# Performance work log

Hardware: AMD Instinct MI355X
Metric: run time of the kernel (lower is better)

Reference implementation:

```python
import jax, jax.numpy as jnp
import numpy as np
from jax import lax

L, H, D, HID, FF, S, B, IN = 2, 8, 64, 512, 2048, 256, 8, 512


def _self_ref(x, Wy, Wq, Wk, wb):
    # x: (B,H,S,D) already softmaxed; Wy/Wq/Wk: (B,H,D,D); wb: (B,H,D,4)
    # Self-referential weight matrix update (SRWM, self_ref_v0):
    #   y = Wy x; q = softmax(Wq x); k = softmax(Wk x); beta = sigmoid(wb^T x)
    #   W <- W + beta_W * (W q - W k) outer k   (one beta per sub-matrix)
    def step(carry, x_t):
        Wy, Wq, Wk, wb = carry
        y = jnp.einsum('bhij,bhj->bhi', Wy, x_t)
        q = jax.nn.softmax(jnp.einsum('bhij,bhj->bhi', Wq, x_t), axis=-1)
        k = jax.nn.softmax(jnp.einsum('bhij,bhj->bhi', Wk, x_t), axis=-1)
        beta = jax.nn.sigmoid(jnp.einsum('bhjc,bhj->bhc', wb, x_t))  # (B,H,4)
        d = q - k                                                    # W q - W k = W (q-k)
        dy = jnp.einsum('bhij,bhj->bhi', Wy, d)
        dq = jnp.einsum('bhij,bhj->bhi', Wq, d)
        dk = jnp.einsum('bhij,bhj->bhi', Wk, d)
        db = jnp.einsum('bhjc,bhj->bhc', wb, d)                      # (B,H,4)
        Wy = Wy + beta[..., 0, None, None] * dy[..., :, None] * k[..., None, :]
        Wq = Wq + beta[..., 1, None, None] * dq[..., :, None] * k[..., None, :]
        Wk = Wk + beta[..., 2, None, None] * dk[..., :, None] * k[..., None, :]
        wb = wb + beta[..., 3, None, None] * k[..., :, None] * db[..., None, :]
        return (Wy, Wq, Wk, wb), y
    xs = jnp.moveaxis(x, 2, 0)  # (S,B,H,D)
    carry, ys = lax.scan(step, (Wy, Wq, Wk, wb), xs)
    return jnp.moveaxis(ys, 0, 2), carry  # (B,H,S,D), final states


def _layernorm(x, g, b):
    mu = x.mean(-1, keepdims=True)
    v = jnp.mean((x - mu) ** 2, axis=-1, keepdims=True)
    return (x - mu) * lax.rsqrt(v + 1e-5) * g + b


def _forward(x, Wy_states, Wq_states, Wk_states, wb_states, in_W, in_b,
             Wy_p, Wq_p, Wk_p, wb_p, Wo, ff_W1, ff_b1, ff_W2, ff_b2, ln_g, ln_b):
    out = x @ in_W.T + in_b  # (S,B,HID)
    sy, sq, sk, sb = [], [], [], []
    for i in range(L):
        h = out
        xs = jax.nn.softmax(h.reshape(S, B, H, D), axis=-1)
        xs = jnp.transpose(xs, (1, 2, 0, 3))  # (B,H,S,D)
        Wy_bc = Wy_states[i] + Wy_p[i][None]
        Wq_bc = Wq_states[i] + Wq_p[i][None]
        Wk_bc = Wk_states[i] + Wk_p[i][None]
        wb_bc = wb_states[i] + wb_p[i][None]
        y, (Wyf, Wqf, Wkf, wbf) = _self_ref(xs, Wy_bc, Wq_bc, Wk_bc, wb_bc)
        o = jnp.transpose(y, (2, 0, 1, 3)).reshape(S, B, H * D) @ Wo[i].T
        out = h + o  # residual (dropout=0)
        sy.append(Wyf - Wy_p[i][None]); sq.append(Wqf - Wq_p[i][None])
        sk.append(Wkf - Wk_p[i][None]); sb.append(wbf - wb_p[i][None])
        # Transformer FF block (pre-LN, residual)
        ln = _layernorm(out, ln_g[i], ln_b[i])
        out = out + jax.nn.relu(ln @ ff_W1[i].T + ff_b1[i]) @ ff_W2[i].T + ff_b2[i]
    return out, jnp.stack(sy), jnp.stack(sq), jnp.stack(sk), jnp.stack(sb)


def setup_inputs() -> dict:
    key = jax.random.key(0)
    ks = jax.random.split(key, 12)
    sd = 1.0 / np.sqrt(D)
    f32 = jnp.float32
    return {
        'x': jax.random.normal(ks[0], (S, B, IN), f32),
        'Wy_states': jnp.zeros((L, B, H, D, D), f32),
        'Wq_states': jnp.zeros((L, B, H, D, D), f32),
        'Wk_states': jnp.zeros((L, B, H, D, D), f32),
        'wb_states': jnp.zeros((L, B, H, D, 4), f32),
        'in_W': jax.random.normal(ks[1], (HID, IN), f32) / np.sqrt(IN),
        'in_b': jnp.zeros((HID,), f32),
        'Wy_p': jax.random.normal(ks[2], (L, H, D, D), f32) * sd,
        'Wq_p': jax.random.normal(ks[3], (L, H, D, D), f32) * sd,
        'Wk_p': jax.random.normal(ks[4], (L, H, D, D), f32) * sd,
        'wb_p': jax.random.normal(ks[5], (L, H, D, 4), f32) * sd,
        'Wo': jax.random.normal(ks[6], (L, HID, HID), f32) / np.sqrt(HID),
        'ff_W1': jax.random.normal(ks[7], (L, FF, HID), f32) / np.sqrt(HID),
        'ff_b1': jnp.zeros((L, FF), f32),
        'ff_W2': jax.random.normal(ks[8], (L, HID, FF), f32) / np.sqrt(FF),
        'ff_b2': jnp.zeros((L, HID), f32),
        'ln_g': jnp.ones((L, HID), f32),
        'ln_b': jnp.zeros((L, HID), f32),
    }


def reference(x, Wy_states, Wq_states, Wk_states, wb_states, in_W, in_b,
              Wy_p, Wq_p, Wk_p, wb_p, Wo, ff_W1, ff_b1, ff_W2, ff_b2, ln_g, ln_b):
    return _forward(x, Wy_states, Wq_states, Wk_states, wb_states, in_W, in_b,
                    Wy_p, Wq_p, Wk_p, wb_p, Wo, ff_W1, ff_b1, ff_W2, ff_b2, ln_g, ln_b)
```

## Files before the change

### kernel.cpp

```cpp
#include <hip/hip_runtime.h>

#define L_NUM 2
#define H_NUM 8
#define D_DIM 64
#define HID_D 512
#define FF_D  2048
#define S_SEQ 256
#define B_NUM 8

typedef unsigned short u16;
typedef unsigned int   u32;
typedef __attribute__((ext_vector_type(8))) short bf16x8;
typedef __attribute__((ext_vector_type(4))) float f32x4;
typedef __attribute__((ext_vector_type(16))) int i32x16;

__device__ __forceinline__ u16 f2bu(float f){
  u32 u = __float_as_uint(f);
  u32 r = (u + 0x7fffu + ((u>>16)&1u)) >> 16;
  return (u16)r;
}

template<int CTL,int RM,int BM>
__device__ __forceinline__ float dpp_add_src(float v){
  return __int_as_float(__builtin_amdgcn_update_dpp(0, __float_as_int(v), CTL, RM, BM, false));
}

__device__ __forceinline__ float wave_sum(float v){
  float t;
  t = dpp_add_src<0x111,0xf,0xf>(v); v += t;
  t = dpp_add_src<0x112,0xf,0xf>(v); v += t;
  t = dpp_add_src<0x114,0xf,0xf>(v); v += t;
  t = dpp_add_src<0x118,0xf,0xf>(v); v += t;
  t = dpp_add_src<0x142,0xa,0xf>(v); v += t;
  t = dpp_add_src<0x143,0xc,0xf>(v); v += t;
  return __int_as_float(__builtin_amdgcn_readlane(__float_as_int(v), 63));
}

__device__ __forceinline__ void wave_sum4(float&a,float&b,float&c,float&d){
  float ta,tb,tc,td;
  ta=dpp_add_src<0x111,0xf,0xf>(a); tb=dpp_add_src<0x111,0xf,0xf>(b);
  tc=dpp_add_src<0x111,0xf,0xf>(c); td=dpp_add_src<0x111,0xf,0xf>(d);
  a+=ta; b+=tb; c+=tc; d+=td;
  ta=dpp_add_src<0x112,0xf,0xf>(a); tb=dpp_add_src<0x112,0xf,0xf>(b);
  tc=dpp_add_src<0x112,0xf,0xf>(c); td=dpp_add_src<0x112,0xf,0xf>(d);
  a+=ta; b+=tb; c+=tc; d+=td;
  ta=dpp_add_src<0x114,0xf,0xf>(a); tb=dpp_add_src<0x114,0xf,0xf>(b);
  tc=dpp_add_src<0x114,0xf,0xf>(c); td=dpp_add_src<0x114,0xf,0xf>(d);
  a+=ta; b+=tb; c+=tc; d+=td;
  ta=dpp_add_src<0x118,0xf,0xf>(a); tb=dpp_add_src<0x118,0xf,0xf>(b);
  tc=dpp_add_src<0x118,0xf,0xf>(c); td=dpp_add_src<0x118,0xf,0xf>(d);
  a+=ta; b+=tb; c+=tc; d+=td;
  ta=dpp_add_src<0x142,0xa,0xf>(a); tb=dpp_add_src<0x142,0xa,0xf>(b);
  tc=dpp_add_src<0x142,0xa,0xf>(c); td=dpp_add_src<0x142,0xa,0xf>(d);
  a+=ta; b+=tb; c+=tc; d+=td;
  ta=dpp_add_src<0x143,0xc,0xf>(a); tb=dpp_add_src<0x143,0xc,0xf>(b);
  tc=dpp_add_src<0x143,0xc,0xf>(c); td=dpp_add_src<0x143,0xc,0xf>(d);
  a+=ta; b+=tb; c+=tc; d+=td;
  a=__int_as_float(__builtin_amdgcn_readlane(__float_as_int(a),63));
  b=__int_as_float(__builtin_amdgcn_readlane(__float_as_int(b),63));
  c=__int_as_float(__builtin_amdgcn_readlane(__float_as_int(c),63));
  d=__int_as_float(__builtin_amdgcn_readlane(__float_as_int(d),63));
}

__device__ __forceinline__ void lds_barrier(){
  __builtin_amdgcn_sched_barrier(0);
  asm volatile("s_waitcnt lgkmcnt(0)" ::: "memory");
  __builtin_amdgcn_s_barrier();
  __builtin_amdgcn_sched_barrier(0);
}

__device__ __forceinline__ void sload_x64(const float* p,
    i32x16& a, i32x16& b, i32x16& c, i32x16& d){
  asm volatile(
    "s_load_dwordx16 %0, %4, 0x0\n\t"
    "s_load_dwordx16 %1, %4, 0x40\n\t"
    "s_load_dwordx16 %2, %4, 0x80\n\t"
    "s_load_dwordx16 %3, %4, 0xC0"
    : "=&s"(a), "=&s"(b), "=&s"(c), "=&s"(d)
    : "s"((unsigned long long)(__SIZE_TYPE__)p));
}

__global__ __launch_bounds__(256) void cvt_bf16_k(
    const float* __restrict__ in, u16* __restrict__ out, int n8)
{
  int i = blockIdx.x*256 + threadIdx.x;
  if (i < n8){
    const float4* p = reinterpret_cast<const float4*>(in + (size_t)i*8);
    float4 v0 = p[0], v1 = p[1];
    u16 t[8] = {f2bu(v0.x),f2bu(v0.y),f2bu(v0.z),f2bu(v0.w),
                f2bu(v1.x),f2bu(v1.y),f2bu(v1.z),f2bu(v1.w)};
    *reinterpret_cast<uint4*>(out + (size_t)i*8) = *reinterpret_cast<uint4*>(t);
  }
}

__global__ __launch_bounds__(256) void softmax_xs_k(
    const float* __restrict__ h, float* __restrict__ xs)
{
  int rid  = blockIdx.x*4 + (threadIdx.x>>6);
  int lane = threadIdx.x & 63;
  int hd = rid & (H_NUM-1);
  int sb = rid >> 3;
  int b  = sb & (B_NUM-1);
  int s  = sb >> 3;
  float v = h[(size_t)sb*HID_D + hd*D_DIM + lane];
  float m = v;
  #pragma unroll
  for (int off=32; off; off>>=1) m = fmaxf(m, __shfl_xor(m, off));
  float e = __expf(v-m);
  float sum = wave_sum(e);
  xs[(((size_t)(b*H_NUM+hd))*S_SEQ + s)*D_DIM + lane] = e/sum;
}

__global__ __launch_bounds__(256,1) void scan4_k(
    const float* __restrict__ xs,
    const float* __restrict__ st_y, const float* __restrict__ st_q,
    const float* __restrict__ st_k, const float* __restrict__ st_b,
    const float* __restrict__ p_y,  const float* __restrict__ p_q,
    const float* __restrict__ p_k,  const float* __restrict__ p_b,
    u16* __restrict__ y_out,
    float* __restrict__ o_sy, float* __restrict__ o_sq,
    float* __restrict__ o_sk, float* __restrict__ o_sb)
{
  const int bh = blockIdx.x;
  const int b  = bh >> 3, hh = bh & 7;
  const int wave = threadIdx.x >> 6, lane = threadIdx.x & 63;

  __shared__ __align__(16) float q_s[2][64];
  __shared__ __align__(16) float k_s[2][64];
  __shared__ float beta_s[2][4];

  float W[64];
  float wb0=0.f, wb1=0.f, wb2=0.f, wb3=0.f;
  float xr[8], xn[8];
  float b3_reg=0.f;
  i32x16 xc0, xc1, xc2, xc3;

  const float* xbase = xs + (size_t)bh * (S_SEQ*D_DIM);

  if (wave < 3) {
    const float* st = (wave==0)? st_y : (wave==1)? st_q : st_k;
    const float* pp = (wave==0)? p_y  : (wave==1)? p_q  : p_k;
    const float4* s4 = reinterpret_cast<const float4*>(st + ((size_t)bh*64 + lane)*64);
    const float4* p4 = reinterpret_cast<const float4*>(pp + ((size_t)hh*64 + lane)*64);
    #pragma unroll
    for (int c=0;c<16;c++){
      float4 a = s4[c], p = p4[c];
      W[c*4+0]=a.x+p.x; W[c*4+1]=a.y+p.y; W[c*4+2]=a.z+p.z; W[c*4+3]=a.w+p.w;
    }
    sload_x64(xbase, xc0, xc1, xc2, xc3);
  } else {
    float4 sv = *reinterpret_cast<const float4*>(st_b + ((size_t)bh*64+lane)*4);
    float4 pv = *reinterpret_cast<const float4*>(p_b  + ((size_t)hh*64+lane)*4);
    wb0 = sv.x+pv.x; wb1 = sv.y+pv.y; wb2 = sv.z+pv.z; wb3 = sv.w+pv.w;
    #pragma unroll
    for (int i=0;i<8;i++) xr[i] = xbase[i*D_DIM + lane];
  }
  __syncthreads();

#define MV16(XV, BASE)                                              \
    _Pragma("unroll")                                               \
    for (int e=0;e<16;e+=4){                                        \
      a0 = fmaf(W[(BASE)+e+0], __int_as_float(XV[e+0]), a0);        \
      a1 = fmaf(W[(BASE)+e+1], __int_as_float(XV[e+1]), a1);        \
      a2 = fmaf(W[(BASE)+e+2], __int_as_float(XV[e+2]), a2);        \
      a3 = fmaf(W[(BASE)+e+3], __int_as_float(XV[e+3]), a3);        \
    }

  for (int t0=0; t0<S_SEQ; t0+=8){
    #pragma unroll
    for (int i=0;i<8;i++){
      const int t = t0 + i;
      const int buf = i & 1;
      if (wave < 3){
        asm volatile("s_waitcnt lgkmcnt(0)" ::: "memory");
        float a0=0.f,a1=0.f,a2=0.f,a3=0.f;
        MV16(xc0, 0)
        MV16(xc1, 16)
        MV16(xc2, 32)
        MV16(xc3, 48)
        float r = (a0+a1)+(a2+a3);
        if (wave==0){
          y_out[((size_t)t*B_NUM + b)*HID_D + hh*D_DIM + lane] = f2bu(r);
        } else {
          float e = __expf(r);
          float s = wave_sum(e);
          float val = e * __builtin_amdgcn_rcpf(s);
          (wave==1 ? q_s[buf] : k_s[buf])[lane] = val;
        }
      } else {
        if (i == 0){
          #pragma unroll
          for (int ii=0;ii<8;ii++){
            const int tt = (t0+8+ii) & (S_SEQ-1);
            xn[ii] = xbase[tt*D_DIM + lane];
          }
        }
        float xl = xr[i];
        float s0 = wb0*xl, s1 = wb1*xl, s2 = wb2*xl, s3 = wb3*xl;
        wave_sum4(s0,s1,s2,s3);
        float bb0 = __builtin_amdgcn_rcpf(1.f+__expf(-s0));
        float bb1 = __builtin_amdgcn_rcpf(1.f+__expf(-s1));
        float bb2 = __builtin_amdgcn_rcpf(1.f+__expf(-s2));
        b3_reg    = __builtin_amdgcn_rcpf(1.f+__expf(-s3));
        if (lane==0){
          beta_s[buf][0]=bb0; beta_s[buf][1]=bb1; beta_s[buf][2]=bb2;
          beta_s[buf][3]=b3_reg;
        }
      }
      lds_barrier();
      if (wave < 3){
        {
          const int tn = (t+1) & (S_SEQ-1);
          sload_x64(xbase + tn*D_DIM, xc0, xc1, xc2, xc3);
        }
        float bw = beta_s[buf][wave];
        float kr[64];
        float a0=0.f,a1=0.f,a2=0.f,a3=0.f;
        #pragma unroll
        for (int j=0;j<16;j++){
          float4 qv = reinterpret_cast<const float4*>(q_s[buf])[j];
          float4 kv = reinterpret_cast<const float4*>(k_s[buf])[j];
          kr[j*4+0]=kv.x; kr[j*4+1]=kv.y; kr[j*4+2]=kv.z; kr[j*4+3]=kv.w;
          a0 = fmaf(W[j*4+0], qv.x-kv.x, a0);
          a1 = fmaf(W[j*4+1], qv.y-kv.y, a1);
          a2 = fmaf(W[j*4+2], qv.z-kv.z, a2);
          a3 = fmaf(W[j*4+3], qv.w-kv.w, a3);
        }
        float rd = (a0+a1)+(a2+a3);
        float cc = bw * rd;
        #pragma unroll
        for (int j=0;j<64;j++)
          W[j] = fmaf(cc, kr[j], W[j]);
      } else {
        float qn = q_s[buf][lane], kn = k_s[buf][lane];
        float dv = qn - kn;
        float d0 = wb0*dv, d1 = wb1*dv, d2 = wb2*dv, d3 = wb3*dv;
        wave_sum4(d0,d1,d2,d3);
        float bk = b3_reg * kn;
        wb0 = fmaf(bk, d0, wb0);
        wb1 = fmaf(bk, d1, wb1);
        wb2 = fmaf(bk, d2, wb2);
        wb3 = fmaf(bk, d3, wb3);
      }
    }
    if (wave == 3){
      #pragma unroll
      for (int i=0;i<8;i++) xr[i] = xn[i];
    }
  }
#undef MV16

  if (wave < 3){
    const float* pp = (wave==0)? p_y : (wave==1)? p_q : p_k;
    float* o = ((wave==0)? o_sy : (wave==1)? o_sq : o_sk) + ((size_t)bh*64 + lane)*64;
    const float4* p4 = reinterpret_cast<const float4*>(pp + ((size_t)hh*64 + lane)*64);
    #pragma unroll
    for (int c=0;c<16;c++){
      float4 p = p4[c];
      float4 w;
      w.x = W[c*4+0]-p.x; w.y = W[c*4+1]-p.y; w.z = W[c*4+2]-p.z; w.w = W[c*4+3]-p.w;
      reinterpret_cast<float4*>(o)[c] = w;
    }
  } else {
    float4 pv = *reinterpret_cast<const float4*>(p_b + ((size_t)hh*64+lane)*4);
    float4 w;
    w.x = wb0-pv.x; w.y = wb1-pv.y; w.z = wb2-pv.z; w.w = wb3-pv.w;
    *reinterpret_cast<float4*>(o_sb + ((size_t)bh*64+lane)*4) = w;
  }
}

template<bool BIAS,bool RELU,bool ADDC,bool OBF>
__global__ __launch_bounds__(256) void mgemm_k(
    const u16* __restrict__ A, const u16* __restrict__ Bw,
    const float* __restrict__ Cin, const float* __restrict__ bias,
    float* __restrict__ Of, u16* __restrict__ Ob,
    int M, int N, int K)
{
  constexpr int BK  = 64;
  constexpr int LDT = 72;
  __shared__ __align__(16) u16 As[128][LDT];
  __shared__ __align__(16) u16 Bs[128][LDT];

  const int tid  = threadIdx.x;
  const int wv   = tid >> 6;
  const int lane = tid & 63;
  const int wr   = (wv >> 1) * 64;
  const int wc   = (wv & 1) * 64;
  const int lr   = lane & 15;
  const int lg   = lane >> 4;
  const int m0 = blockIdx.y * 128, n0 = blockIdx.x * 128;

  const int sr = tid >> 1;
  const int sk = (tid & 1) * 32;

  f32x4 acc[4][4] = {};

  for (int kt = 0; kt < K; kt += BK){
    {
      const uint4* src = reinterpret_cast<const uint4*>(A + (size_t)(m0+sr)*K + kt + sk);
      uint4 v0=src[0], v1=src[1], v2=src[2], v3=src[3];
      uint4* dst = reinterpret_cast<uint4*>(&As[sr][sk]);
      dst[0]=v0; dst[1]=v1; dst[2]=v2; dst[3]=v3;
    }
    {
      const uint4* src = reinterpret_cast<const uint4*>(Bw + (size_t)(n0+sr)*K + kt + sk);
      uint4 v0=src[0], v1=src[1], v2=src[2], v3=src[3];
      uint4* dst = reinterpret_cast<uint4*>(&Bs[sr][sk]);
      dst[0]=v0; dst[1]=v1; dst[2]=v2; dst[3]=v3;
    }
    __syncthreads();

    #pragma unroll
    for (int half=0; half<2; ++half){
      bf16x8 af[4], bfb[4];
      #pragma unroll
      for (int i=0;i<4;i++)
        af[i]  = *reinterpret_cast<const bf16x8*>(&As[wr + i*16 + lr][half*32 + lg*8]);
      #pragma unroll
      for (int j=0;j<4;j++)
        bfb[j] = *reinterpret_cast<const bf16x8*>(&Bs[wc + j*16 + lr][half*32 + lg*8]);
      #pragma unroll
      for (int i=0;i<4;i++)
        #pragma unroll
        for (int j=0;j<4;j++)
          acc[i][j] = __builtin_amdgcn_mfma_f32_16x16x32_bf16(af[i], bfb[j], acc[i][j], 0,0,0);
    }
    __syncthreads();
  }

  #pragma unroll
  for (int j=0;j<4;j++){
    const int col = n0 + wc + j*16 + lr;
    float bv = 0.f;
    if (BIAS) bv = bias[col];
    #pragma unroll
    for (int i=0;i<4;i++){
      const int rbase = m0 + wr + i*16 + lg*4;
      #pragma unroll
      for (int dj=0;dj<4;dj++){
        const int row = rbase + dj;
        float v = acc[i][j][dj];
        if (BIAS) v += bv;
        if (ADDC) v += Cin[(size_t)row*N + col];
        if (RELU) v = fmaxf(v, 0.f);
        if (OBF) Ob[(size_t)row*N + col] = f2bu(v);
        else     Of[(size_t)row*N + col] = v;
      }
    }
  }
}

__global__ __launch_bounds__(256) void ln_k(
    const float* __restrict__ h, const float* __restrict__ g,
    const float* __restrict__ bb, u16* __restrict__ out)
{
  int row  = blockIdx.x*4 + (threadIdx.x>>6);
  int lane = threadIdx.x & 63;
  const float4* hr = reinterpret_cast<const float4*>(h + (size_t)row*HID_D) + lane*2;
  float4 u = hr[0], v = hr[1];
  float vals[8] = {u.x,u.y,u.z,u.w,v.x,v.y,v.z,v.w};
  float s = 0.f;
  #pragma unroll
  for (int e=0;e<8;e++) s += vals[e];
  s = wave_sum(s);
  float mu = s * (1.f/HID_D);
  float vs = 0.f;
  #pragma unroll
  for (int e=0;e<8;e++){ float d = vals[e]-mu; vs += d*d; }
  vs = wave_sum(vs);
  float rs = rsqrtf(vs*(1.f/HID_D) + 1e-5f);
  const float4* gr = reinterpret_cast<const float4*>(g) + lane*2;
  const float4* br = reinterpret_cast<const float4*>(bb) + lane*2;
  float4 g0 = gr[0], g1 = gr[1], b0 = br[0], b1 = br[1];
  u16 ov[8];
  ov[0] = f2bu((vals[0]-mu)*rs*g0.x + b0.x);
  ov[1] = f2bu((vals[1]-mu)*rs*g0.y + b0.y);
  ov[2] = f2bu((vals[2]-mu)*rs*g0.z + b0.z);
  ov[3] = f2bu((vals[3]-mu)*rs*g0.w + b0.w);
  ov[4] = f2bu((vals[4]-mu)*rs*g1.x + b1.x);
  ov[5] = f2bu((vals[5]-mu)*rs*g1.y + b1.y);
  ov[6] = f2bu((vals[6]-mu)*rs*g1.z + b1.z);
  ov[7] = f2bu((vals[7]-mu)*rs*g1.w + b1.w);
  *reinterpret_cast<uint4*>(out + (size_t)row*HID_D + lane*8) =
      *reinterpret_cast<uint4*>(ov);
}

extern "C" void kernel_launch(void* const* d_in, const int* in_sizes, int n_in,
                              void* d_out, int out_size, void* d_ws, size_t ws_size,
                              hipStream_t stream)
{
  const float* x    = (const float*)d_in[0];
  const float* sty  = (const float*)d_in[1];
  const float* stq  = (const float*)d_in[2];
  const float* stk  = (const float*)d_in[3];
  const float* stb  = (const float*)d_in[4];
  const float* inW  = (const float*)d_in[5];
  const float* inb  = (const float*)d_in[6];
  const float* py   = (const float*)d_in[7];
  const float* pq   = (const float*)d_in[8];
  const float* pk   = (const float*)d_in[9];
  const float* pb   = (const float*)d_in[10];
  const float* Wo   = (const float*)d_in[11];
  const float* fw1  = (const float*)d_in[12];
  const float* fb1  = (const float*)d_in[13];
  const float* fw2  = (const float*)d_in[14];
  const float* fb2  = (const float*)d_in[15];
  const float* lng  = (const float*)d_in[16];
  const float* lnb  = (const float*)d_in[17];

  char* ws = (char*)d_ws;
  float* h    = (float*)ws;
  float* xsb  = (float*)(ws + (4<<20));
  u16*   yb   = (u16*)  (ws + (8<<20));
  u16*   t0   = (u16*)  (ws + (10<<20));
  u16*   t1   = (u16*)  (ws + (12<<20));
  u16*   xb   = (u16*)  (ws + (20<<20));
  u16*   inWb = (u16*)  (ws + (22<<20));
  u16*   Wob  = (u16*)  (ws + (22<<20) + (512*1024));
  u16*   fw1b = (u16*)  (ws + (23<<20) + (512*1024));
  u16*   fw2b = (u16*)  (ws + (27<<20) + (512*1024));

  float* out0 = (float*)d_out;
  const size_t OUT_SZ = (size_t)S_SEQ*B_NUM*HID_D;
  const size_t SYL    = (size_t)B_NUM*H_NUM*D_DIM*D_DIM;
  const size_t SBL    = (size_t)B_NUM*H_NUM*D_DIM*4;
  float* o_sy = out0 + OUT_SZ;
  float* o_sq = o_sy + L_NUM*SYL;
  float* o_sk = o_sq + L_NUM*SYL;
  float* o_sb = o_sk + L_NUM*SYL;

  const int M = S_SEQ*B_NUM;

  cvt_bf16_k<<<512, 256,0,stream>>>(x,   xb,   M*512/8);
  cvt_bf16_k<<<128, 256,0,stream>>>(inW, inWb, 512*512/8);
  cvt_bf16_k<<<256, 256,0,stream>>>(Wo,  Wob,  L_NUM*512*512/8);
  cvt_bf16_k<<<1024,256,0,stream>>>(fw1, fw1b, L_NUM*FF_D*HID_D/8);
  cvt_bf16_k<<<1024,256,0,stream>>>(fw2, fw2b, L_NUM*HID_D*FF_D/8);

  mgemm_k<true,false,false,false><<<dim3(HID_D/128, M/128),256,0,stream>>>(
      xb, inWb, nullptr, inb, h, nullptr, M, HID_D, 512);

  for (int l=0;l<L_NUM;l++){
    softmax_xs_k<<<(S_SEQ*B_NUM*H_NUM)/4, 256, 0, stream>>>(h, xsb);

    scan4_k<<<B_NUM*H_NUM, 256, 0, stream>>>(xsb,
        sty + (size_t)l*SYL, stq + (size_t)l*SYL, stk + (size_t)l*SYL, stb + (size_t)l*SBL,
        py + (size_t)l*H_NUM*D_DIM*D_DIM, pq + (size_t)l*H_NUM*D_DIM*D_DIM,
        pk + (size_t)l*H_NUM*D_DIM*D_DIM, pb + (size_t)l*H_NUM*D_DIM*4,
        yb,
        o_sy + l*SYL, o_sq + l*SYL, o_sk + l*SYL, o_sb + l*SBL);

    mgemm_k<false,false,true,false><<<dim3(HID_D/128, M/128),256,0,stream>>>(
        yb, Wob + (size_t)l*HID_D*HID_D, h, nullptr, h, nullptr, M, HID_D, HID_D);

    ln_k<<<M/4,256,0,stream>>>(h, lng + l*HID_D, lnb + l*HID_D, t0);

    mgemm_k<true,true,false,true><<<dim3(FF_D/128, M/128),256,0,stream>>>(
        t0, fw1b + (size_t)l*FF_D*HID_D, nullptr, fb1 + l*FF_D, nullptr, t1, M, FF_D, HID_D);

    float* dst = (l==L_NUM-1) ? out0 : h;
    mgemm_k<true,false,true,false><<<dim3(HID_D/128, M/128),256,0,stream>>>(
        t1, fw2b + (size_t)l*HID_D*FF_D, h, fb2 + l*HID_D, dst, nullptr, M, HID_D, FF_D);
  }
}
```

Before: 762.0 us.

## Pack two independent scan chains per 512-thread block

The SRWM scan kernel now runs two (batch, head) chains in one 512-thread block, with each group of four waves handling one chain. Shared buffers gain a chain index, and the launch uses half as many blocks. This uses fewer CUs, each running two chains, which may improve latency hiding through interleaving, but the block-wide barrier now couples both chains and they compete for one CU's issue slots.

Result: slower. 1.063 ms (+39.6%).

```diff
diff --git a/kernel.cpp b/kernel.cpp
--- a/kernel.cpp
+++ b/kernel.cpp
@@ -111,7 +111,7 @@
   xs[(((size_t)(b*H_NUM+hd))*S_SEQ + s)*D_DIM + lane] = e/sum;
 }
 
-__global__ __launch_bounds__(256,1) void scan4_k(
+__global__ __launch_bounds__(512,1) void scan8_k(
     const float* __restrict__ xs,
     const float* __restrict__ st_y, const float* __restrict__ st_q,
     const float* __restrict__ st_k, const float* __restrict__ st_b,
@@ -121,13 +121,15 @@
     float* __restrict__ o_sy, float* __restrict__ o_sq,
     float* __restrict__ o_sk, float* __restrict__ o_sb)
 {
-  const int bh = blockIdx.x;
+  const int wave = threadIdx.x >> 6, lane = threadIdx.x & 63;
+  const int chain = __builtin_amdgcn_readfirstlane(wave >> 2);
+  const int role  = wave & 3;
+  const int bh = blockIdx.x*2 + chain;
   const int b  = bh >> 3, hh = bh & 7;
-  const int wave = threadIdx.x >> 6, lane = threadIdx.x & 63;
-
-  __shared__ __align__(16) float q_s[2][64];
-  __shared__ __align__(16) float k_s[2][64];
-  __shared__ float beta_s[2][4];
+
+  __shared__ __align__(16) float q_s[2][2][64];
+  __shared__ __align__(16) float k_s[2][2][64];
+  __shared__ float beta_s[2][2][4];
 
   float W[64];
   float wb0=0.f, wb1=0.f, wb2=0.f, wb3=0.f;
@@ -137,9 +139,9 @@
 
   const float* xbase = xs + (size_t)bh * (S_SEQ*D_DIM);
 
-  if (wave < 3) {
-    const float* st = (wave==0)? st_y : (wave==1)? st_q : st_k;
-    const float* pp = (wave==0)? p_y  : (wave==1)? p_q  : p_k;
+  if (role < 3) {
+    const float* st = (role==0)? st_y : (role==1)? st_q : st_k;
+    const float* pp = (role==0)? p_y  : (role==1)? p_q  : p_k;
     const float4* s4 = reinterpret_cast<const float4*>(st + ((size_t)bh*64 + lane)*64);
     const float4* p4 = reinterpret_cast<const float4*>(pp + ((size_t)hh*64 + lane)*64);
     #pragma unroll
@@ -171,7 +173,7 @@
     for (int i=0;i<8;i++){
       const int t = t0 + i;
       const int buf = i & 1;
-      if (wave < 3){
+      if (role < 3){
         asm volatile("s_waitcnt lgkmcnt(0)" ::: "memory");
         float a0=0.f,a1=0.f,a2=0.f,a3=0.f;
         MV16(xc0, 0)
@@ -179,13 +181,13 @@
         MV16(xc2, 32)
         MV16(xc3, 48)
         float r = (a0+a1)+(a2+a3);
-        if (wave==0){
+        if (role==0){
           y_out[((size_t)t*B_NUM + b)*HID_D + hh*D_DIM + lane] = f2bu(r);
         } else {
           float e = __expf(r);
           float s = wave_sum(e);
           float val = e * __builtin_amdgcn_rcpf(s);
-          (wave==1 ? q_s[buf] : k_s[buf])[lane] = val;
+          (role==1 ? q_s[chain][buf] : k_s[chain][buf])[lane] = val;
         }
       } else {
         if (i == 0){
@@ -203,23 +205,23 @@
         float bb2 = __builtin_amdgcn_rcpf(1.f+__expf(-s2));
         b3_reg    = __builtin_amdgcn_rcpf(1.f+__expf(-s3));
         if (lane==0){
-          beta_s[buf][0]=bb0; beta_s[buf][1]=bb1; beta_s[buf][2]=bb2;
-          beta_s[buf][3]=b3_reg;
+          beta_s[chain][buf][0]=bb0; beta_s[chain][buf][1]=bb1;
+          beta_s[chain][buf][2]=bb2; beta_s[chain][buf][3]=b3_reg;
         }
       }
       lds_barrier();
-      if (wave < 3){
+      if (role < 3){
         {
           const int tn = (t+1) & (S_SEQ-1);
           sload_x64(xbase + tn*D_DIM, xc0, xc1, xc2, xc3);
         }
-        float bw = beta_s[buf][wave];
+        float bw = beta_s[chain][buf][role];
         float kr[64];
         float a0=0.f,a1=0.f,a2=0.f,a3=0.f;
         #pragma unroll
         for (int j=0;j<16;j++){
-          float4 qv = reinterpret_cast<const float4*>(q_s[buf])[j];
-          float4 kv = reinterpret_cast<const float4*>(k_s[buf])[j];
+          float4 qv = reinterpret_cast<const float4*>(q_s[chain][buf])[j];
+          float4 kv = reinterpret_cast<const float4*>(k_s[chain][buf])[j];
           kr[j*4+0]=kv.x; kr[j*4+1]=kv.y; kr[j*4+2]=kv.z; kr[j*4+3]=kv.w;
           a0 = fmaf(W[j*4+0], qv.x-kv.x, a0);
           a1 = fmaf(W[j*4+1], qv.y-kv.y, a1);
@@ -232,7 +234,7 @@
         for (int j=0;j<64;j++)
           W[j] = fmaf(cc, kr[j], W[j]);
       } else {
-        float qn = q_s[buf][lane], kn = k_s[buf][lane];
+        float qn = q_s[chain][buf][lane], kn = k_s[chain][buf][lane];
         float dv = qn - kn;
         float d0 = wb0*dv, d1 = wb1*dv, d2 = wb2*dv, d3 = wb3*dv;
         wave_sum4(d0,d1,d2,d3);
@@ -243,16 +245,16 @@
         wb3 = fmaf(bk, d3, wb3);
       }
     }
-    if (wave == 3){
+    if (role == 3){
       #pragma unroll
       for (int i=0;i<8;i++) xr[i] = xn[i];
     }
   }
 #undef MV16
 
-  if (wave < 3){
-    const float* pp = (wave==0)? p_y : (wave==1)? p_q : p_k;
-    float* o = ((wave==0)? o_sy : (wave==1)? o_sq : o_sk) + ((size_t)bh*64 + lane)*64;
+  if (role < 3){
+    const float* pp = (role==0)? p_y : (role==1)? p_q : p_k;
+    float* o = ((role==0)? o_sy : (role==1)? o_sq : o_sk) + ((size_t)bh*64 + lane)*64;
     const float4* p4 = reinterpret_cast<const float4*>(pp + ((size_t)hh*64 + lane)*64);
     #pragma unroll
     for (int c=0;c<16;c++){
@@ -443,7 +445,7 @@
   for (int l=0;l<L_NUM;l++){
     softmax_xs_k<<<(S_SEQ*B_NUM*H_NUM)/4, 256, 0, stream>>>(h, xsb);
 
-    scan4_k<<<B_NUM*H_NUM, 256, 0, stream>>>(xsb,
+    scan8_k<<<(B_NUM*H_NUM)/2, 512, 0, stream>>>(xsb,
         sty + (size_t)l*SYL, stq + (size_t)l*SYL, stk + (size_t)l*SYL, stb + (size_t)l*SBL,
         py + (size_t)l*H_NUM*D_DIM*D_DIM, pq + (size_t)l*H_NUM*D_DIM*D_DIM,
         pk + (size_t)l*H_NUM*D_DIM*D_DIM, pb + (size_t)l*H_NUM*D_DIM*4,
```
